# Kernel tuning notes

Measured on AMD Instinct MI355X. Metric: run time of the kernel, lower is better.

The kernel has to match this reference:

```python
import jax, jax.numpy as jnp
import numpy as np

B, N = 16384, 4096
NBLOCKS = 4
BLK = N // NBLOCKS  # 1024


def setup_inputs() -> dict:
    key = jax.random.key(0)
    kx, k1, k2, kb = jax.random.split(key, 4)
    # match torch kaiming-style uniform bounds approximately; exact init values
    # don't affect correctness testing, scale kept modest for stability
    bound_w = float(np.sqrt(3.0) * (np.sqrt(2.0 / (1 + 5)) / np.sqrt(BLK)))
    bound_b = 1.0 / float(np.sqrt(N))
    x = jax.random.normal(kx, (B, N), dtype=jnp.float32)
    w1 = jax.random.uniform(k1, (NBLOCKS, BLK, BLK), jnp.float32, -bound_w, bound_w)
    w2 = jax.random.uniform(k2, (NBLOCKS, BLK, BLK), jnp.float32, -bound_w, bound_w)
    bias = jax.random.uniform(kb, (N,), jnp.float32, -bound_b, bound_b)
    return {"x": x, "w1": w1, "w2": w2, "bias": bias}


def monarch_matmul(x, w1, w2):
    # x: (B, n); w1: (k, q, p) with k*p = n; w2: (l, s, r) with l*r = k*q
    Bd, n = x.shape
    k, q, p = w1.shape
    l, s, r = w2.shape
    # out1[b,k,q] = sum_p x[b,k,p] * w1[k,q,p]
    out1 = jnp.einsum('bkp,kqp->bkq', x.reshape(Bd, k, p), w1)
    # permute (k*q) flat -> (r, l), then transpose to (l, r)
    t = out1.reshape(Bd, r, l).transpose(0, 2, 1)  # (B, l, r)
    # out2[b,l,s] = sum_r t[b,l,r] * w2[l,s,r]
    out2 = jnp.einsum('blr,lsr->bls', t, w2)
    # permute to (B, s, l) then flatten -> (B, s*l)
    return out2.transpose(0, 2, 1).reshape(Bd, s * l)


def reference(x, w1, w2, bias):
    return monarch_matmul(x, w1, w2) + bias
```

## Files before the change

### kernel.cpp

```cpp
#include <hip/hip_runtime.h>
#include <hip/hip_bf16.h>
#include <stdint.h>

typedef __bf16 bf16_t;
typedef bf16_t bf16x8 __attribute__((ext_vector_type(8)));
typedef bf16_t bf16x4 __attribute__((ext_vector_type(4)));
typedef float  f32x4  __attribute__((ext_vector_type(4)));

#define B_DIM 16384

#define BARM()   do { asm volatile("" ::: "memory"); \
                      __builtin_amdgcn_s_barrier();  \
                      asm volatile("" ::: "memory"); } while (0)
#define MEMF()   asm volatile("" ::: "memory")
#define VMCNT6() asm volatile("s_waitcnt vmcnt(6)" ::: "memory")
#define VMCNT0() asm volatile("s_waitcnt vmcnt(0)" ::: "memory")

__device__ __forceinline__ void async_copy16(void* lptr, const void* gptr) {
  __builtin_amdgcn_global_load_lds(
      (const __attribute__((address_space(1))) unsigned int*)gptr,
      (__attribute__((address_space(3))) unsigned int*)lptr, 16, 0, 0);
}

__global__ void cast_all_kernel(const float* __restrict__ x, const float* __restrict__ w1,
                                const float* __restrict__ w2, bf16_t* __restrict__ xb,
                                bf16_t* __restrict__ w1b, bf16_t* __restrict__ w2b) {
  size_t c = (size_t)blockIdx.x * 256 + threadIdx.x;
  const float* s; bf16_t* d; size_t off;
  if (c < 8388608)      { s = x;  d = xb;  off = c; }
  else if (c < 8912896) { s = w1; d = w1b; off = c - 8388608; }
  else                  { s = w2; d = w2b; off = c - 8912896; }
  size_t i = off * 8;
  f32x4 a = *(const f32x4*)(s + i);
  f32x4 b = *(const f32x4*)(s + i + 4);
  bf16x8 o;
  o[0]=(bf16_t)a[0]; o[1]=(bf16_t)a[1]; o[2]=(bf16_t)a[2]; o[3]=(bf16_t)a[3];
  o[4]=(bf16_t)b[0]; o[5]=(bf16_t)b[1]; o[6]=(bf16_t)b[2]; o[7]=(bf16_t)b[3];
  *(bf16x8*)(d + i) = o;
}

template<int EPI>
__global__ __launch_bounds__(512, 2)
void monarch_gemm8(const bf16_t* __restrict__ Ab, const bf16_t* __restrict__ Wb,
                   bf16_t* __restrict__ Outb)
{
  __shared__ __align__(16) char smem[131072];
  const int tid  = threadIdx.x;
  const int lane = tid & 63;
  const int wid  = tid >> 6;
  const int wm   = wid >> 2;
  const int wn   = wid & 3;

  const int pb = blockIdx.x;
  const int lb = (pb & 7) * 128 + (pb >> 3);
  const int zi = lb >> 8;
  const int mt = (lb & 255) >> 2;
  const int nt = lb & 3;

  const size_t brow0 = (size_t)mt * 256;
  const int    ncol0 = nt * 256;

  const bf16_t* Asrc = Ab + brow0 * 4096 + (size_t)zi * 1024;
  const bf16_t* Bsrc = Wb + ((size_t)zi << 20) + (size_t)ncol0 * 1024;

  const int sRow = lane >> 3;
  const int sC   = (lane & 7) ^ sRow;

#define STAGE(BUF, T, H) do {                                                   \
    const bf16_t* _s = (H) < 2 ? Asrc + ((size_t)((H) * 128) * 4096) + (T) * 64 \
                               : Bsrc + ((size_t)(((H)-2) * 128) * 1024) + (T) * 64; \
    const size_t _st = (H) < 2 ? 4096 : 1024;                                   \
    async_copy16(smem + (BUF)*65536 + ((H)>>1)*32768 + ((H)&1)*16384 + wid*1024,\
                 _s + (size_t)(wid * 8 + sRow) * _st + sC * 8);                 \
    async_copy16(smem + (BUF)*65536 + ((H)>>1)*32768 + ((H)&1)*16384 + 8192 + wid*1024, \
                 _s + (size_t)(64 + wid * 8 + sRow) * _st + sC * 8);            \
  } while (0)

  const int cs0 = ((0 + (lane >> 4)) ^ (lane & 7)) * 16;
  const int cs1 = ((4 + (lane >> 4)) ^ (lane & 7)) * 16;
  const int aBase = (wm * 128 + (lane & 15)) * 128;
  const int bBase = 32768 + (wn * 64 + (lane & 15)) * 128;

#define RDA(buf, m, kk) (*(const bf16x8*)(smem + (buf)*65536 + aBase + (m)*2048 + ((kk)?cs1:cs0)))
#define RDB(buf, n, kk) (*(const bf16x8*)(smem + (buf)*65536 + bBase + (n)*2048 + ((kk)?cs1:cs0)))

  f32x4 acc[8][4] = {};
  bf16x8 aM0[4][2], aM1[4][2], bN0[2][2], bN1[2][2];

#define MFMA_QUAD(AR, Aarr, NB, Barr)                                              \
  __builtin_amdgcn_s_setprio(1);                                                   \
  _Pragma("unroll") for (int m = 0; m < 4; ++m)                                    \
  _Pragma("unroll") for (int n = 0; n < 2; ++n)                                    \
  _Pragma("unroll") for (int kk = 0; kk < 2; ++kk)                                 \
    acc[(AR)+m][(NB)+n] = __builtin_amdgcn_mfma_f32_16x16x32_bf16(                 \
        Aarr[m][kk], Barr[n][kk], acc[(AR)+m][(NB)+n], 0, 0, 0);                   \
  __builtin_amdgcn_s_setprio(0);

#define LD_A0(buf) _Pragma("unroll") for (int m = 0; m < 4; ++m) { \
    aM0[m][0] = RDA(buf,m,0); aM0[m][1] = RDA(buf,m,1); }
#define LD_A1(buf) _Pragma("unroll") for (int m = 0; m < 4; ++m) { \
    aM1[m][0] = RDA(buf,m+4,0); aM1[m][1] = RDA(buf,m+4,1); }
#define LD_B0(buf) _Pragma("unroll") for (int n = 0; n < 2; ++n) { \
    bN0[n][0] = RDB(buf,n,0); bN0[n][1] = RDB(buf,n,1); }
#define LD_B1(buf) _Pragma("unroll") for (int n = 0; n < 2; ++n) { \
    bN1[n][0] = RDB(buf,n+2,0); bN1[n][1] = RDB(buf,n+2,1); }

  STAGE(0,0,0); MEMF(); STAGE(0,0,1); MEMF(); STAGE(0,0,2); MEMF(); STAGE(0,0,3); MEMF();
  STAGE(1,1,0); MEMF(); STAGE(1,1,1); MEMF(); STAGE(1,1,2);
  VMCNT6(); BARM();

  for (int it2 = 0; it2 < 8; ++it2) {
    const int t0 = it2 * 2;
    const bool nl = (it2 < 7);
    LD_A0(0); LD_B0(0);
    MEMF(); STAGE(1, t0+1, 3);
    BARM();
    MFMA_QUAD(0, aM0, 0, bN0);
    LD_A1(0);
    BARM();
    MFMA_QUAD(4, aM1, 0, bN0);
    LD_B1(0);
    if (nl) { MEMF(); STAGE(0, t0+2, 0); }
    BARM();
    MFMA_QUAD(0, aM0, 2, bN1);
    if (nl) { MEMF(); STAGE(0, t0+2, 1); MEMF(); STAGE(0, t0+2, 2); VMCNT6(); }
    else    { VMCNT0(); }
    BARM();
    MFMA_QUAD(4, aM1, 2, bN1);
    LD_A0(1); LD_B0(1);
    if (nl) { MEMF(); STAGE(0, t0+2, 3); }
    BARM();
    MFMA_QUAD(0, aM0, 0, bN0);
    LD_A1(1);
    BARM();
    MFMA_QUAD(4, aM1, 0, bN0);
    LD_B1(1);
    if (nl) { MEMF(); STAGE(1, t0+3, 0); }
    BARM();
    MFMA_QUAD(0, aM0, 2, bN1);
    if (nl) { MEMF(); STAGE(1, t0+3, 1); MEMF(); STAGE(1, t0+3, 2); VMCNT6(); }
    BARM();
    MFMA_QUAD(4, aM1, 2, bN1);
  }

  if (EPI == 0) {
    bf16_t* C0 = (bf16_t*)smem;
    #pragma unroll
    for (int half = 0; half < 2; ++half) {
      BARM();
      if (wm == half) {
        const int rg = lane >> 4, cl = lane & 15;
        const int l = cl & 3, rvb = cl >> 2;
        #pragma unroll
        for (int m = 0; m < 8; ++m)
          #pragma unroll
          for (int n = 0; n < 4; ++n) {
            const int rowb = (m * 16 + rg * 4) * 288 + l * 72 + wn * 16 + n * 4 + rvb;
            #pragma unroll
            for (int j = 0; j < 4; ++j)
              C0[rowb + j * 288] = (bf16_t)acc[m][n][j];
          }
      }
      BARM();
      #pragma unroll
      for (int i = 0; i < 8; ++i) {
        const int s = i * 512 + tid;
        const int row = s >> 5, l2 = (s >> 3) & 3, part = s & 7;
        bf16x8 v = *(const bf16x8*)&C0[row * 288 + l2 * 72 + part * 8];
        *(bf16x8*)&Outb[(brow0 + half * 128 + row) * 4096 +
                        l2 * 1024 + zi * 256 + nt * 64 + part * 8] = v;
      }
    }
  } else {
    bf16_t* C = (bf16_t*)smem;
    #pragma unroll
    for (int half = 0; half < 2; ++half) {
      BARM();
      if (wm == half) {
        const int rg = lane >> 4, cl = lane & 15;
        #pragma unroll
        for (int m = 0; m < 8; ++m)
          #pragma unroll
          for (int n = 0; n < 4; ++n) {
            const int rl = m * 16 + rg * 4;
            const int col = wn * 64 + n * 16 + cl;
            #pragma unroll
            for (int j = 0; j < 4; ++j)
              C[(rl + j) * 264 + col] = (bf16_t)acc[m][n][j];
          }
      }
      BARM();
      #pragma unroll
      for (int i = 0; i < 8; ++i) {
        const int s = i * 512 + tid;
        const int row = s >> 5, ch = s & 31;
        bf16x8 v = *(const bf16x8*)&C[row * 264 + ch * 8];
        *(bf16x8*)&Outb[(brow0 + half * 128 + row) * 4096 +
                        (size_t)zi * 1024 + ncol0 + ch * 8] = v;
      }
    }
  }
#undef RDA
#undef RDB
#undef MFMA_QUAD
#undef LD_A0
#undef LD_A1
#undef LD_B0
#undef LD_B1
#undef STAGE
}

__global__ void permute_bias_kernel(const bf16_t* __restrict__ o2,
                                    const float* __restrict__ bias,
                                    float* __restrict__ out) {
  const int t = blockIdx.x * 256 + threadIdx.x;
  const int b = t >> 8;
  const int s0 = (t & 255) * 4;
  const size_t rowb = (size_t)b * 4096;
  bf16x4 vl[4];
  #pragma unroll
  for (int l = 0; l < 4; ++l) vl[l] = *(const bf16x4*)(o2 + rowb + l * 1024 + s0);
  #pragma unroll
  for (int si = 0; si < 4; ++si) {
    f32x4 bb = *(const f32x4*)(bias + (size_t)(s0 + si) * 4);
    f32x4 o;
    o[0] = (float)vl[0][si] + bb[0];
    o[1] = (float)vl[1][si] + bb[1];
    o[2] = (float)vl[2][si] + bb[2];
    o[3] = (float)vl[3][si] + bb[3];
    *(f32x4*)(out + rowb + (size_t)(s0 + si) * 4) = o;
  }
}

extern "C" void kernel_launch(void* const* d_in, const int* in_sizes, int n_in,
                              void* d_out, int out_size, void* d_ws, size_t ws_size,
                              hipStream_t stream) {
  const float* x    = (const float*)d_in[0];
  const float* w1   = (const float*)d_in[1];
  const float* w2   = (const float*)d_in[2];
  const float* bias = (const float*)d_in[3];
  float* out = (float*)d_out;

  char* ws = (char*)d_ws;
  const size_t xbBytes    = (size_t)B_DIM * 4096 * 2;
  const size_t wBytes     = (size_t)8 << 20;
  bf16_t* xb    = (bf16_t*)(ws);
  bf16_t* w1b   = (bf16_t*)(ws + xbBytes);
  bf16_t* w2b   = (bf16_t*)(ws + xbBytes + wBytes);
  bf16_t* inter = (bf16_t*)(ws + xbBytes + 2 * wBytes);
  bf16_t* o2    = xb;

  cast_all_kernel<<<36864, 256, 0, stream>>>(x, w1, w2, xb, w1b, w2b);
  monarch_gemm8<0><<<1024, 512, 0, stream>>>(xb, w1b, inter);
  monarch_gemm8<1><<<1024, 512, 0, stream>>>(inter, w2b, o2);
  permute_bias_kernel<<<16384, 256, 0, stream>>>(o2, bias, out);
}
```

Measured before the change: 473.1 us.

## Fuse output permute and bias add into second GEMM epilogue

Removes the separate permute+bias kernel by having the second GEMM write fp32 output directly in the final permuted layout with bias staged in LDS. The bf16 intermediate write and re-read of o2 go away, along with one kernel launch. The block-to-tile mapping for the second GEMM is also reordered so the four zi blocks of the same rows run adjacently. The fused stores are scalar fp32 writes with stride 4 across columns, so they may coalesce poorly compared with the old vectorized writes.

```diff
diff --git a/kernel.cpp b/kernel.cpp
--- a/kernel.cpp
+++ b/kernel.cpp
@@ -42,7 +42,8 @@
 template<int EPI>
 __global__ __launch_bounds__(512, 2)
 void monarch_gemm8(const bf16_t* __restrict__ Ab, const bf16_t* __restrict__ Wb,
-                   bf16_t* __restrict__ Outb)
+                   bf16_t* __restrict__ Outb, float* __restrict__ Outf,
+                   const float* __restrict__ bias)
 {
   __shared__ __align__(16) char smem[131072];
   const int tid  = threadIdx.x;
@@ -53,9 +54,9 @@
 
   const int pb = blockIdx.x;
   const int lb = (pb & 7) * 128 + (pb >> 3);
-  const int zi = lb >> 8;
-  const int mt = (lb & 255) >> 2;
-  const int nt = lb & 3;
+  int zi, mt, nt;
+  if (EPI == 0) { zi = lb >> 8;  mt = (lb & 255) >> 2; nt = lb & 3; }
+  else          { zi = lb & 3;   nt = (lb >> 2) & 3;   mt = lb >> 4; }
 
   const size_t brow0 = (size_t)mt * 256;
   const int    ncol0 = nt * 256;
@@ -173,6 +174,7 @@
     }
   } else {
     bf16_t* C = (bf16_t*)smem;
+    float*  biasLds = (float*)(smem + 69632);
     #pragma unroll
     for (int half = 0; half < 2; ++half) {
       BARM();
@@ -189,14 +191,24 @@
               C[(rl + j) * 264 + col] = (bf16_t)acc[m][n][j];
           }
       }
+      if (half == 0 && tid < 256)
+        biasLds[tid] = bias[(size_t)(ncol0 + tid) * 4 + zi];
       BARM();
       #pragma unroll
       for (int i = 0; i < 8; ++i) {
-        const int s = i * 512 + tid;
-        const int row = s >> 5, ch = s & 31;
+        const int c = i * 512 + tid;
+        const int row = c >> 5, ch = c & 31;
         bf16x8 v = *(const bf16x8*)&C[row * 264 + ch * 8];
-        *(bf16x8*)&Outb[(brow0 + half * 128 + row) * 4096 +
-                        (size_t)zi * 1024 + ncol0 + ch * 8] = v;
+        f32x4 b0 = *(const f32x4*)&biasLds[ch * 8];
+        f32x4 b1 = *(const f32x4*)&biasLds[ch * 8 + 4];
+        const size_t rowOff = (brow0 + half * 128 + row) * 4096;
+        const size_t sbase  = (size_t)(ncol0 + ch * 8) * 4 + zi;
+        #pragma unroll
+        for (int u = 0; u < 4; ++u)
+          Outf[rowOff + sbase + u * 4] = (float)v[u] + b0[u];
+        #pragma unroll
+        for (int u = 0; u < 4; ++u)
+          Outf[rowOff + sbase + (u + 4) * 4] = (float)v[u + 4] + b1[u];
       }
     }
   }
@@ -210,28 +222,6 @@
 #undef STAGE
 }
 
-__global__ void permute_bias_kernel(const bf16_t* __restrict__ o2,
-                                    const float* __restrict__ bias,
-                                    float* __restrict__ out) {
-  const int t = blockIdx.x * 256 + threadIdx.x;
-  const int b = t >> 8;
-  const int s0 = (t & 255) * 4;
-  const size_t rowb = (size_t)b * 4096;
-  bf16x4 vl[4];
-  #pragma unroll
-  for (int l = 0; l < 4; ++l) vl[l] = *(const bf16x4*)(o2 + rowb + l * 1024 + s0);
-  #pragma unroll
-  for (int si = 0; si < 4; ++si) {
-    f32x4 bb = *(const f32x4*)(bias + (size_t)(s0 + si) * 4);
-    f32x4 o;
-    o[0] = (float)vl[0][si] + bb[0];
-    o[1] = (float)vl[1][si] + bb[1];
-    o[2] = (float)vl[2][si] + bb[2];
-    o[3] = (float)vl[3][si] + bb[3];
-    *(f32x4*)(out + rowb + (size_t)(s0 + si) * 4) = o;
-  }
-}
-
 extern "C" void kernel_launch(void* const* d_in, const int* in_sizes, int n_in,
                               void* d_out, int out_size, void* d_ws, size_t ws_size,
                               hipStream_t stream) {
@@ -248,10 +238,8 @@
   bf16_t* w1b   = (bf16_t*)(ws + xbBytes);
   bf16_t* w2b   = (bf16_t*)(ws + xbBytes + wBytes);
   bf16_t* inter = (bf16_t*)(ws + xbBytes + 2 * wBytes);
-  bf16_t* o2    = xb;
 
   cast_all_kernel<<<36864, 256, 0, stream>>>(x, w1, w2, xb, w1b, w2b);
-  monarch_gemm8<0><<<1024, 512, 0, stream>>>(xb, w1b, inter);
-  monarch_gemm8<1><<<1024, 512, 0, stream>>>(inter, w2b, o2);
-  permute_bias_kernel<<<16384, 256, 0, stream>>>(o2, bias, out);
-}
+  monarch_gemm8<0><<<1024, 512, 0, stream>>>(xb, w1b, inter, nullptr, nullptr);
+  monarch_gemm8<1><<<1024, 512, 0, stream>>>(inter, w2b, nullptr, out, bias);
+}
```

New measurement: 602.7 us. 27.4% more time.
